# Kernel optimization log

Hardware: AMD Instinct MI355X
Metric: run time of the kernel (lower is better)

The kernel has to match this reference:

```python
import jax, jax.numpy as jnp
import numpy as np

NP_PEP, NP_PROT = 50000, 8000
E, EL = 1_600_000, 200_000
F_IN, H = 1280, 128


def _mean_aggr(x_src, src_idx, dst_idx, n_dst):
    # gather source feats per edge, scatter-mean into destination nodes
    msg = jax.ops.segment_sum(x_src[src_idx], dst_idx, num_segments=n_dst)  # [n_dst, H]
    deg = jax.ops.segment_sum(jnp.ones((src_idx.shape[0], 1), x_src.dtype), dst_idx, num_segments=n_dst)
    return msg / jnp.maximum(deg, 1.0)


def _hetero_sage(x_pep, x_prot, e_src, e_dst,
                 Wl_b, Wr_b, b_b, Wl_r, Wr_r, b_r):
    # edge type pep->prot (bind): updates prot nodes
    m_prot = _mean_aggr(x_pep, e_src, e_dst, x_prot.shape[0])
    out_prot = m_prot @ Wl_b + x_prot @ Wr_b + b_b
    # edge type prot->pep (rev_bind): updates pep nodes
    m_pep = _mean_aggr(x_prot, e_dst, e_src, x_pep.shape[0])
    out_pep = m_pep @ Wl_r + x_pep @ Wr_r + b_r
    return out_pep, out_prot


def setup_inputs() -> dict:
    key = jax.random.key(0)
    ks = jax.random.split(key, 24)
    s = 0.02
    inp = {
        'x_pep': jax.random.normal(ks[0], (NP_PEP, F_IN), jnp.float32),
        'x_prot': jax.random.normal(ks[1], (NP_PROT, F_IN), jnp.float32),
        'e_src': jax.random.randint(ks[2], (E,), 0, NP_PEP, jnp.int32),
        'e_dst': jax.random.randint(ks[3], (E,), 0, NP_PROT, jnp.int32),
        'el_src': jax.random.randint(ks[4], (EL,), 0, NP_PEP, jnp.int32),
        'el_dst': jax.random.randint(ks[5], (EL,), 0, NP_PROT, jnp.int32),
        'W_pep': s * jax.random.normal(ks[6], (F_IN, H), jnp.float32),
        'b_pep': jnp.zeros((H,), jnp.float32),
        'W_prot': s * jax.random.normal(ks[7], (F_IN, H), jnp.float32),
        'b_prot': jnp.zeros((H,), jnp.float32),
    }
    names = ['Wl1_bind', 'Wr1_bind', 'Wl1_rev', 'Wr1_rev',
             'Wl2_bind', 'Wr2_bind', 'Wl2_rev', 'Wr2_rev']
    for i, n in enumerate(names):
        inp[n] = s * jax.random.normal(ks[8 + i], (H, H), jnp.float32)
    for n in ['b1_bind', 'b1_rev', 'b2_bind', 'b2_rev']:
        inp[n] = jnp.zeros((H,), jnp.float32)
    return inp


def reference(x_pep, x_prot, e_src, e_dst, el_src, el_dst,
              W_pep, b_pep, W_prot, b_prot,
              Wl1_bind, Wr1_bind, b1_bind, Wl1_rev, Wr1_rev, b1_rev,
              Wl2_bind, Wr2_bind, b2_bind, Wl2_rev, Wr2_rev, b2_rev):
    # input projections (pep_emb/prot_emb unused in original forward)
    h_pep = x_pep @ W_pep + b_pep      # [NP_PEP, H]
    h_prot = x_prot @ W_prot + b_prot  # [NP_PROT, H]
    # SAGE layer 1 + relu
    h_pep, h_prot = _hetero_sage(h_pep, h_prot, e_src, e_dst,
                                 Wl1_bind, Wr1_bind, b1_bind,
                                 Wl1_rev, Wr1_rev, b1_rev)
    h_pep, h_prot = jax.nn.relu(h_pep), jax.nn.relu(h_prot)
    # SAGE layer 2
    h_pep, h_prot = _hetero_sage(h_pep, h_prot, e_src, e_dst,
                                 Wl2_bind, Wr2_bind, b2_bind,
                                 Wl2_rev, Wr2_rev, b2_rev)
    # classifier: edge-indexed gather + dot product
    return (h_pep[el_src] * h_prot[el_dst]).sum(axis=-1)  # [EL]
```

## Files before the change

### kernel.cpp

```cpp
#include <hip/hip_runtime.h>
#include <hip/hip_bf16.h>
#include <cstdint>

#define NP_PEP 50000
#define NP_PROT 8000
#define NE 1600000
#define NEL 200000
#define F_IN 1280
#define HDIM 128

#define CHUNK 4096
#define NBLK 391
#define NBQ 500
#define SHQ 4
#define NPBQ 16
#define NBP 391
#define SHP 7
#define NPBP 128

#define PROJ_BLK_PEP 391
#define PROJ_BLK_PROT 63
#define AGG_BLK_PROT 2000
#define AGG_BLK_PEP 12500

typedef __attribute__((ext_vector_type(8))) short bfrag;
typedef __attribute__((ext_vector_type(4))) short bhalf4;
typedef __attribute__((ext_vector_type(4))) float f32x4;

__device__ __forceinline__ ushort f2bf(float x) {
    __hip_bfloat16 h = __float2bfloat16(x);
    ushort u;
    __builtin_memcpy(&u, &h, 2);
    return u;
}
__device__ inline void unpack2(uint u, float& lo, float& hi) {
    union { uint u; float f; } a, b;
    a.u = u << 16; b.u = u & 0xffff0000u;
    lo = a.f; hi = b.f;
}
__device__ inline uint pack2(float a, float b) {
    return (uint)f2bf(a) | ((uint)f2bf(b) << 16);
}

__device__ __forceinline__ void cp16_g2l(const void* g, void* l) {
    __builtin_amdgcn_global_load_lds(
        (const __attribute__((address_space(1))) void*)g,
        (__attribute__((address_space(3))) void*)l, 16, 0, 0);
}


__global__ __launch_bounds__(512) void bin_count(const int* __restrict__ esrc,
                                                 const int* __restrict__ edst,
                                                 int* __restrict__ Gq,
                                                 int* __restrict__ Gp) {
    __shared__ int hq[NBQ];
    __shared__ int hp[NBP];
    int b = blockIdx.x, t = threadIdx.x;
    if (t < NBQ) hq[t] = 0;
    if (t < NBP) hp[t] = 0;
    __syncthreads();
    int e0 = b * CHUNK, cnt = min(CHUNK, NE - e0);
#pragma unroll
    for (int r = 0; r < 8; ++r) {
        int i = t + r * 512;
        if (i < cnt) {
            atomicAdd(&hq[edst[e0 + i] >> SHQ], 1);
            atomicAdd(&hp[esrc[e0 + i] >> SHP], 1);
        }
    }
    __syncthreads();
    if (t < NBQ) Gq[t * NBLK + b] = hq[t];
    if (t < NBP) Gp[t * NBLK + b] = hp[t];
}

__global__ __launch_bounds__(512) void rel_offsets(const int* __restrict__ Gq,
                                                   int* __restrict__ Oq, int* __restrict__ Tq,
                                                   const int* __restrict__ Gp,
                                                   int* __restrict__ Op, int* __restrict__ Tp) {
    const int* G; int* O; int* T; int j;
    if (blockIdx.x < NBQ) { G = Gq; O = Oq; T = Tq; j = blockIdx.x; }
    else                  { G = Gp; O = Op; T = Tp; j = blockIdx.x - NBQ; }
    __shared__ int sh[512];
    int t = threadIdx.x;
    int v = (t < NBLK) ? G[j * NBLK + t] : 0;
    sh[t] = v;
    __syncthreads();
    for (int off = 1; off < 512; off <<= 1) {
        int a = sh[t];
        int c = (t >= off) ? sh[t - off] : 0;
        __syncthreads();
        sh[t] = a + c;
        __syncthreads();
    }
    if (t < NBLK) O[j * NBLK + t] = sh[t] - v;
    if (t == 511) T[j] = sh[511];
}

__global__ __launch_bounds__(512) void base_scan(const int* __restrict__ Tq, int* __restrict__ Bq,
                                                 const int* __restrict__ Tp, int* __restrict__ Bp) {
    __shared__ int sh[512];
    int t = threadIdx.x;
    int v = (t < NBQ) ? Tq[t] : 0;
    sh[t] = v;
    __syncthreads();
    for (int off = 1; off < 512; off <<= 1) {
        int a = sh[t];
        int c = (t >= off) ? sh[t - off] : 0;
        __syncthreads();
        sh[t] = a + c;
        __syncthreads();
    }
    if (t < NBQ) Bq[t] = sh[t] - v;
    if (t == 0) Bq[NBQ] = NE;
    __syncthreads();
    int v2 = (t < NBP) ? Tp[t] : 0;
    sh[t] = v2;
    __syncthreads();
    for (int off = 1; off < 512; off <<= 1) {
        int a = sh[t];
        int c = (t >= off) ? sh[t - off] : 0;
        __syncthreads();
        sh[t] = a + c;
        __syncthreads();
    }
    if (t < NBP) Bp[t] = sh[t] - v2;
    if (t == 0) Bp[NBP] = NE;
}

__global__ __launch_bounds__(512) void bin_scatter2(const int* __restrict__ esrc,
                                                    const int* __restrict__ edst,
                                                    const int* __restrict__ Oq,
                                                    const int* __restrict__ Bq,
                                                    const int* __restrict__ Op,
                                                    const int* __restrict__ Bp,
                                                    uint* __restrict__ stagQ,
                                                    uint* __restrict__ stagP) {
    __shared__ int hist[512];
    __shared__ int start[512];
    __shared__ uint sorted[CHUNK];
    int b = blockIdx.x, t = threadIdx.x;
    int e0 = b * CHUNK, cnt = min(CHUNK, NE - e0);
    uint pk[8];
    bool val[8];
#pragma unroll
    for (int r = 0; r < 8; ++r) {
        int i = t + r * 512;
        val[r] = (i < cnt);
        if (val[r]) {
            int s = esrc[e0 + i], d = edst[e0 + i];
            pk[r] = ((uint)s << 13) | (uint)d;
        }
    }
    for (int dir = 0; dir < 2; ++dir) {
        const int* O = dir ? Op : Oq;
        const int* B = dir ? Bp : Bq;
        uint* stg = dir ? stagP : stagQ;
        int shf = dir ? SHP : SHQ;
        hist[t] = 0;
        __syncthreads();
        int bk[8];
#pragma unroll
        for (int r = 0; r < 8; ++r) {
            bk[r] = -1;
            if (val[r]) {
                int key = dir ? (int)(pk[r] >> 13) : (int)(pk[r] & 8191u);
                bk[r] = key >> shf;
                atomicAdd(&hist[bk[r]], 1);
            }
        }
        __syncthreads();
        int ownv = hist[t];
        start[t] = ownv;
        __syncthreads();
        for (int off = 1; off < 512; off <<= 1) {
            int a = start[t];
            int c = (t >= off) ? start[t - off] : 0;
            __syncthreads();
            start[t] = a + c;
            __syncthreads();
        }
        int excl = start[t] - ownv;
        start[t] = excl;
        hist[t] = excl;
        __syncthreads();
#pragma unroll
        for (int r = 0; r < 8; ++r)
            if (bk[r] >= 0) {
                int rank = atomicAdd(&hist[bk[r]], 1);
                sorted[rank] = pk[r];
            }
        __syncthreads();
#pragma unroll
        for (int r = 0; r < 8; ++r) {
            int i = t + r * 512;
            if (i < cnt) {
                uint v = sorted[i];
                int key = dir ? (int)(v >> 13) : (int)(v & 8191u);
                int bb = key >> shf;
                stg[B[bb] + O[bb * NBLK + b] + (i - start[bb])] = v;
            }
        }
        __syncthreads();
    }
}

__global__ __launch_bounds__(256) void finalize_csr(const uint* __restrict__ stagQ,
                                                    const int* __restrict__ Bq,
                                                    int* __restrict__ rowptr_prot,
                                                    int* __restrict__ col_prot,
                                                    const uint* __restrict__ stagP,
                                                    const int* __restrict__ Bp,
                                                    int* __restrict__ rowptr_pep,
                                                    int* __restrict__ col_pep) {
    __shared__ int cnts[128];
    __shared__ int sc[128];
    __shared__ int cur[128];
    const uint* stg; const int* B; int* rowptr; int* col;
    int n, npb, j, use_dst;
    if (blockIdx.x < NBQ) {
        stg = stagQ; B = Bq; rowptr = rowptr_prot; col = col_prot;
        n = NP_PROT; npb = NPBQ; j = blockIdx.x; use_dst = 1;
    } else {
        stg = stagP; B = Bp; rowptr = rowptr_pep; col = col_pep;
        n = NP_PEP; npb = NPBP; j = blockIdx.x - NBQ; use_dst = 0;
    }
    int t = threadIdx.x;
    int first = j * npb;
    int nn = min(npb, n - first);
    if (t < 128) cnts[t] = 0;
    __syncthreads();
    int s0 = B[j], s1 = B[j + 1];
    for (int i = s0 + t; i < s1; i += 256) {
        uint v = stg[i];
        int key = use_dst ? (int)(v & 8191u) : (int)(v >> 13);
        atomicAdd(&cnts[key - first], 1);
    }
    __syncthreads();
    int v = 0;
    if (t < 128) { v = cnts[t]; sc[t] = v; }
    __syncthreads();
    for (int off = 1; off < 128; off <<= 1) {
        int a = 0, c = 0;
        if (t < 128) { a = sc[t]; c = (t >= off) ? sc[t - off] : 0; }
        __syncthreads();
        if (t < 128) sc[t] = a + c;
        __syncthreads();
    }
    if (t < nn) {
        int excl = sc[t] - v;
        rowptr[first + t] = s0 + excl;
        cur[t] = s0 + excl;
    }
    if (t == 0 && j == 0) rowptr[n] = NE;
    __syncthreads();
    for (int i = s0 + t; i < s1; i += 256) {
        uint v2 = stg[i];
        int key, pay;
        if (use_dst) { key = (int)(v2 & 8191u); pay = (int)(v2 >> 13); }
        else         { key = (int)(v2 >> 13);   pay = (int)(v2 & 8191u); }
        int pos = atomicAdd(&cur[key - first], 1);
        col[pos] = pay;
    }
}


#define WST_TILE 4096

__global__ __launch_bounds__(256) void wprep(const float* __restrict__ Wp,
                                             const float* __restrict__ Wq,
                                             const float* __restrict__ m0,
                                             const float* __restrict__ m1,
                                             const float* __restrict__ m2,
                                             const float* __restrict__ m3,
                                             const float* __restrict__ m4,
                                             const float* __restrict__ m5,
                                             const float* __restrict__ m6,
                                             const float* __restrict__ m7,
                                             ushort* __restrict__ out) {
    int b = blockIdx.x;
    const float* W; int kt; size_t base;
    if (b < 40)      { W = Wp; kt = b;       base = 0; }
    else if (b < 80) { W = Wq; kt = b - 40;  base = (size_t)40 * WST_TILE; }
    else {
        int mm = (b - 80) >> 2; kt = (b - 80) & 3;
        switch (mm) {
            case 0: W = m0; break; case 1: W = m1; break;
            case 2: W = m2; break; case 3: W = m3; break;
            case 4: W = m4; break; case 5: W = m5; break;
            case 6: W = m6; break; default: W = m7; break;
        }
        base = (size_t)(80 + 4 * mm) * WST_TILE;
    }
    int t = threadIdx.x;
#pragma unroll
    for (int r = 0; r < 2; ++r) {
        int idx = t + r * 256;
        int n = ((idx >> 6) << 4) | (idx & 15);
        int h = (idx >> 4) & 3;
        const float* wp = W + (size_t)(kt * 32 + h * 8) * HDIM + n;
        bfrag p;
#pragma unroll
        for (int j = 0; j < 8; ++j) p[j] = (short)f2bf(wp[(size_t)j * HDIM]);
        *(bfrag*)&out[base + (size_t)kt * WST_TILE + (size_t)idx * 8] = p;
    }
}

__global__ __launch_bounds__(256) void gemm_proj2(const float* __restrict__ Aa,
                                                  const ushort* __restrict__ Wsta,
                                                  const float* __restrict__ ba,
                                                  ushort* __restrict__ Ca, int Ma, int nblk_a,
                                                  const float* __restrict__ Ab,
                                                  const ushort* __restrict__ Wstb,
                                                  const float* __restrict__ bb,
                                                  ushort* __restrict__ Cb, int Mb) {
    __shared__ ushort Alds[4096];
    __shared__ ushort Blds[4096];
    __shared__ ushort Clds[128 * 136];
    const float* A; const ushort* Wst; const float* bias; ushort* Cg; int M, blk;
    if ((int)blockIdx.x < nblk_a) { A = Aa; Wst = Wsta; bias = ba; Cg = Ca; M = Ma; blk = blockIdx.x; }
    else                          { A = Ab; Wst = Wstb; bias = bb; Cg = Cb; M = Mb; blk = blockIdx.x - nblk_a; }
    int tid = threadIdx.x;
    int lane = tid & 63, w = tid >> 6, wm = w >> 1, wn = w & 1;
    int r0 = blk * 128;

    f32x4 acc[4][4];
#pragma unroll
    for (int i = 0; i < 4; ++i)
#pragma unroll
        for (int j = 0; j < 4; ++j) acc[i][j] = (f32x4){0.f, 0.f, 0.f, 0.f};

    for (int kt = 0; kt < F_IN / 32; ++kt) {
        int k0 = kt * 32;
        const ushort* wsrc = Wst + (size_t)kt * WST_TILE;
        cp16_g2l(wsrc + (size_t)tid * 8, &Blds[(size_t)tid * 8]);
        cp16_g2l(wsrc + 2048 + (size_t)tid * 8, &Blds[2048 + (size_t)tid * 8]);
#pragma unroll
        for (int i = 0; i < 4; ++i) {
            int idx = tid + 256 * i;
            int row = idx >> 3, q = idx & 7;
            int gr = min(r0 + row, M - 1);
            float4 v = *(const float4*)(A + (size_t)gr * F_IN + k0 + q * 4);
            bhalf4 p;
            p.x = (short)f2bf(v.x); p.y = (short)f2bf(v.y);
            p.z = (short)f2bf(v.z); p.w = (short)f2bf(v.w);
            int off = ((row >> 4) * 64 + ((q >> 1) << 4) + (row & 15)) * 8 + (q & 1) * 4;
            *(bhalf4*)&Alds[off] = p;
        }
        __syncthreads();
        const bfrag* Af = (const bfrag*)Alds;
        const bfrag* Bf = (const bfrag*)Blds;
        bfrag af[4], bf_[4];
#pragma unroll
        for (int i = 0; i < 4; ++i) af[i] = Af[(wm * 4 + i) * 64 + lane];
#pragma unroll
        for (int j = 0; j < 4; ++j) bf_[j] = Bf[(wn * 4 + j) * 64 + lane];
#pragma unroll
        for (int i = 0; i < 4; ++i)
#pragma unroll
            for (int j = 0; j < 4; ++j)
                acc[i][j] = __builtin_amdgcn_mfma_f32_16x16x32_bf16(af[i], bf_[j], acc[i][j], 0, 0, 0);
        __syncthreads();
    }
#pragma unroll
    for (int j = 0; j < 4; ++j) {
        int colL = wn * 64 + j * 16 + (lane & 15);
        float bcol = bias[colL];
#pragma unroll
        for (int i = 0; i < 4; ++i) {
            int rbase = wm * 64 + i * 16 + ((lane >> 4) << 2);
            f32x4 v = acc[i][j];
            Clds[(rbase + 0) * 136 + colL] = f2bf(v.x + bcol);
            Clds[(rbase + 1) * 136 + colL] = f2bf(v.y + bcol);
            Clds[(rbase + 2) * 136 + colL] = f2bf(v.z + bcol);
            Clds[(rbase + 3) * 136 + colL] = f2bf(v.w + bcol);
        }
    }
    __syncthreads();
#pragma unroll
    for (int c = 0; c < 8; ++c) {
        int cidx = c * 256 + tid;
        int row = cidx >> 4, h = cidx & 15;
        int gr = r0 + row;
        if (gr < M)
            *(bfrag*)(Cg + (size_t)gr * HDIM + h * 8) = *(const bfrag*)&Clds[row * 136 + h * 8];
    }
}

__global__ __launch_bounds__(256) void lin2f(const ushort* A1a, const ushort* W1a,
                                             const ushort* A2a, const ushort* W2a,
                                             const float* __restrict__ ba,
                                             ushort* Ca, int Ma, int nblk_a,
                                             const ushort* A1b, const ushort* W1b,
                                             const ushort* A2b, const ushort* W2b,
                                             const float* __restrict__ bb,
                                             ushort* Cb, int Mb, int do_relu) {
    __shared__ ushort Alds[4096];
    __shared__ ushort Blds[4096];
    __shared__ ushort Clds[128 * 136];
    const ushort *A1, *A2, *W1, *W2; const float* bias; ushort* C; int M, blk;
    if ((int)blockIdx.x < nblk_a) {
        A1 = A1a; W1 = W1a; A2 = A2a; W2 = W2a; bias = ba; C = Ca; M = Ma; blk = blockIdx.x;
    } else {
        A1 = A1b; W1 = W1b; A2 = A2b; W2 = W2b; bias = bb; C = Cb; M = Mb; blk = blockIdx.x - nblk_a;
    }
    int tid = threadIdx.x;
    int lane = tid & 63, w = tid >> 6, wm = w >> 1, wn = w & 1;
    int r0 = blk * 128;

    int arow = ((tid >> 6) << 4) | (tid & 15);
    int ah = (tid >> 4) & 3;
    int gr1 = min(r0 + arow, M - 1);
    int gr2 = min(r0 + arow + 64, M - 1);

    f32x4 acc[4][4];
#pragma unroll
    for (int i = 0; i < 4; ++i)
#pragma unroll
        for (int j = 0; j < 4; ++j) acc[i][j] = (f32x4){0.f, 0.f, 0.f, 0.f};

    for (int kt = 0; kt < 8; ++kt) {
        const ushort* A = (kt < 4) ? A1 : A2;
        const ushort* Wt = (kt < 4) ? W1 : W2;
        int k0 = (kt & 3) * 32;
        cp16_g2l(A + (size_t)gr1 * HDIM + k0 + ah * 8, &Alds[(size_t)tid * 8]);
        cp16_g2l(A + (size_t)gr2 * HDIM + k0 + ah * 8, &Alds[(size_t)(tid + 256) * 8]);
        const ushort* wsrc = Wt + (size_t)(kt & 3) * WST_TILE;
        cp16_g2l(wsrc + (size_t)tid * 8, &Blds[(size_t)tid * 8]);
        cp16_g2l(wsrc + 2048 + (size_t)tid * 8, &Blds[2048 + (size_t)tid * 8]);
        __syncthreads();
        const bfrag* Af = (const bfrag*)Alds;
        const bfrag* Bf = (const bfrag*)Blds;
        bfrag af[4], bf_[4];
#pragma unroll
        for (int i = 0; i < 4; ++i) af[i] = Af[(wm * 4 + i) * 64 + lane];
#pragma unroll
        for (int j = 0; j < 4; ++j) bf_[j] = Bf[(wn * 4 + j) * 64 + lane];
#pragma unroll
        for (int i = 0; i < 4; ++i)
#pragma unroll
            for (int j = 0; j < 4; ++j)
                acc[i][j] = __builtin_amdgcn_mfma_f32_16x16x32_bf16(af[i], bf_[j], acc[i][j], 0, 0, 0);
        __syncthreads();
    }
#pragma unroll
    for (int j = 0; j < 4; ++j) {
        int colL = wn * 64 + j * 16 + (lane & 15);
        float bcol = bias[colL];
#pragma unroll
        for (int i = 0; i < 4; ++i) {
            int rbase = wm * 64 + i * 16 + ((lane >> 4) << 2);
            f32x4 v = acc[i][j];
            float o0 = v.x + bcol, o1 = v.y + bcol, o2 = v.z + bcol, o3 = v.w + bcol;
            if (do_relu) {
                o0 = fmaxf(o0, 0.f); o1 = fmaxf(o1, 0.f);
                o2 = fmaxf(o2, 0.f); o3 = fmaxf(o3, 0.f);
            }
            Clds[(rbase + 0) * 136 + colL] = f2bf(o0);
            Clds[(rbase + 1) * 136 + colL] = f2bf(o1);
            Clds[(rbase + 2) * 136 + colL] = f2bf(o2);
            Clds[(rbase + 3) * 136 + colL] = f2bf(o3);
        }
    }
    __syncthreads();
#pragma unroll
    for (int c = 0; c < 8; ++c) {
        int cidx = c * 256 + tid;
        int row = cidx >> 4, h = cidx & 15;
        int gr = r0 + row;
        if (gr < M)
            *(bfrag*)(C + (size_t)gr * HDIM + h * 8) = *(const bfrag*)&Clds[row * 136 + h * 8];
    }
}

__global__ __launch_bounds__(256) void aggr2(const ushort* __restrict__ Ha,
                                             const int* __restrict__ rpa,
                                             const int* __restrict__ cola,
                                             ushort* __restrict__ Oa, int Na, int nblk_a,
                                             const ushort* __restrict__ Hb,
                                             const int* __restrict__ rpb,
                                             const int* __restrict__ colb,
                                             ushort* __restrict__ Ob, int Nb) {
    const ushort* H; const int* rp; const int* col; ushort* O; int N, blk;
    if ((int)blockIdx.x < nblk_a) { H = Ha; rp = rpa; col = cola; O = Oa; N = Na; blk = blockIdx.x; }
    else                          { H = Hb; rp = rpb; col = colb; O = Ob; N = Nb; blk = blockIdx.x - nblk_a; }
    int node = blk * 4 + (threadIdx.x >> 6);
    if (node >= N) return;
    int lane = threadIdx.x & 63;
    int sub = lane >> 4;
    int ch = lane & 15;
    int beg = rp[node], end = rp[node + 1];
    int deg = end - beg;
    float a0 = 0, a1 = 0, a2 = 0, a3 = 0, a4 = 0, a5 = 0, a6 = 0, a7 = 0;
    int j = beg + sub;
    for (; j + 4 < end; j += 8) {
        int i0 = col[j], i1 = col[j + 4];
        uint4 u0 = *(const uint4*)(H + (size_t)i0 * HDIM + ch * 8);
        uint4 u1 = *(const uint4*)(H + (size_t)i1 * HDIM + ch * 8);
        float lo, hi;
        unpack2(u0.x, lo, hi); a0 += lo; a1 += hi;
        unpack2(u0.y, lo, hi); a2 += lo; a3 += hi;
        unpack2(u0.z, lo, hi); a4 += lo; a5 += hi;
        unpack2(u0.w, lo, hi); a6 += lo; a7 += hi;
        unpack2(u1.x, lo, hi); a0 += lo; a1 += hi;
        unpack2(u1.y, lo, hi); a2 += lo; a3 += hi;
        unpack2(u1.z, lo, hi); a4 += lo; a5 += hi;
        unpack2(u1.w, lo, hi); a6 += lo; a7 += hi;
    }
    if (j < end) {
        int i0 = col[j];
        uint4 u0 = *(const uint4*)(H + (size_t)i0 * HDIM + ch * 8);
        float lo, hi;
        unpack2(u0.x, lo, hi); a0 += lo; a1 += hi;
        unpack2(u0.y, lo, hi); a2 += lo; a3 += hi;
        unpack2(u0.z, lo, hi); a4 += lo; a5 += hi;
        unpack2(u0.w, lo, hi); a6 += lo; a7 += hi;
    }
    a0 += __shfl_xor(a0, 16); a0 += __shfl_xor(a0, 32);
    a1 += __shfl_xor(a1, 16); a1 += __shfl_xor(a1, 32);
    a2 += __shfl_xor(a2, 16); a2 += __shfl_xor(a2, 32);
    a3 += __shfl_xor(a3, 16); a3 += __shfl_xor(a3, 32);
    a4 += __shfl_xor(a4, 16); a4 += __shfl_xor(a4, 32);
    a5 += __shfl_xor(a5, 16); a5 += __shfl_xor(a5, 32);
    a6 += __shfl_xor(a6, 16); a6 += __shfl_xor(a6, 32);
    a7 += __shfl_xor(a7, 16); a7 += __shfl_xor(a7, 32);
    if (sub == 0) {
        float inv = 1.0f / (float)max(deg, 1);
        uint4 o;
        o.x = pack2(a0 * inv, a1 * inv);
        o.y = pack2(a2 * inv, a3 * inv);
        o.z = pack2(a4 * inv, a5 * inv);
        o.w = pack2(a6 * inv, a7 * inv);
        *(uint4*)(O + (size_t)node * HDIM + ch * 8) = o;
    }
}

__global__ __launch_bounds__(256) void classify_bf16(const ushort* __restrict__ hp,
                                                     const ushort* __restrict__ hr,
                                                     const int* __restrict__ esrc,
                                                     const int* __restrict__ edst,
                                                     float* __restrict__ out, int n) {
    int t = blockIdx.x * blockDim.x + threadIdx.x;
    int edge = t >> 4;
    int ch = t & 15;
    if (edge >= n) return;
    int s = esrc[edge], d = edst[edge];
    uint4 ua = *(const uint4*)(hp + (size_t)s * HDIM + ch * 8);
    uint4 ub = *(const uint4*)(hr + (size_t)d * HDIM + ch * 8);
    float al, ah, bl, bh;
    float v = 0.f;
    unpack2(ua.x, al, ah); unpack2(ub.x, bl, bh); v += al * bl + ah * bh;
    unpack2(ua.y, al, ah); unpack2(ub.y, bl, bh); v += al * bl + ah * bh;
    unpack2(ua.z, al, ah); unpack2(ub.z, bl, bh); v += al * bl + ah * bh;
    unpack2(ua.w, al, ah); unpack2(ub.w, bl, bh); v += al * bl + ah * bh;
    v += __shfl_xor(v, 8);
    v += __shfl_xor(v, 4);
    v += __shfl_xor(v, 2);
    v += __shfl_xor(v, 1);
    if (ch == 0) out[edge] = v;
}


extern "C" void kernel_launch(void* const* d_in, const int* in_sizes, int n_in,
                              void* d_out, int out_size, void* d_ws, size_t ws_size,
                              hipStream_t stream) {
    const float* x_pep   = (const float*)d_in[0];
    const float* x_prot  = (const float*)d_in[1];
    const int*   e_src   = (const int*)d_in[2];
    const int*   e_dst   = (const int*)d_in[3];
    const int*   el_src  = (const int*)d_in[4];
    const int*   el_dst  = (const int*)d_in[5];
    const float* W_pep   = (const float*)d_in[6];
    const float* b_pep   = (const float*)d_in[7];
    const float* W_prot  = (const float*)d_in[8];
    const float* b_prot  = (const float*)d_in[9];
    const float* Wl1_bind = (const float*)d_in[10];
    const float* Wr1_bind = (const float*)d_in[11];
    const float* Wl1_rev  = (const float*)d_in[12];
    const float* Wr1_rev  = (const float*)d_in[13];
    const float* Wl2_bind = (const float*)d_in[14];
    const float* Wr2_bind = (const float*)d_in[15];
    const float* Wl2_rev  = (const float*)d_in[16];
    const float* Wr2_rev  = (const float*)d_in[17];
    const float* b1_bind  = (const float*)d_in[18];
    const float* b1_rev   = (const float*)d_in[19];
    const float* b2_bind  = (const float*)d_in[20];
    const float* b2_rev   = (const float*)d_in[21];
    float* out = (float*)d_out;

    ushort* P0 = (ushort*)d_ws;
    ushort* P1 = P0 + (size_t)NP_PEP * HDIM;
    ushort* R0 = P1 + (size_t)NP_PEP * HDIM;
    ushort* R1 = R0 + (size_t)NP_PROT * HDIM;
    int* rowptr_pep  = (int*)(R1 + (size_t)NP_PROT * HDIM);
    int* rowptr_prot = rowptr_pep + NP_PEP + 1;
    int* col_pep     = rowptr_prot + NP_PROT + 1;
    int* col_prot    = col_pep + NE;
    uint* stagP      = (uint*)(col_prot + NE);
    uint* stagQ      = stagP + NE;
    int* Gq          = (int*)(stagQ + NE);
    int* Oq          = Gq + NBQ * NBLK;
    int* Gp          = Oq + NBQ * NBLK;
    int* Op          = Gp + NBP * NBLK;
    int* Tq          = Op + NBP * NBLK;
    int* Tp          = Tq + NBQ;
    int* Bq          = Tp + NBP;
    int* Bp          = Bq + NBQ + 1;
    uintptr_t wraw   = (uintptr_t)(Bp + NBP + 1);
    ushort* Wst      = (ushort*)((wraw + 255) & ~(uintptr_t)255);

    const ushort* WstPep  = Wst;
    const ushort* WstProt = Wst + (size_t)40 * WST_TILE;
    const ushort* WstL1b  = Wst + (size_t)(80 + 0)  * WST_TILE;
    const ushort* WstR1b  = Wst + (size_t)(80 + 4)  * WST_TILE;
    const ushort* WstL1r  = Wst + (size_t)(80 + 8)  * WST_TILE;
    const ushort* WstR1r  = Wst + (size_t)(80 + 12) * WST_TILE;
    const ushort* WstL2b  = Wst + (size_t)(80 + 16) * WST_TILE;
    const ushort* WstR2b  = Wst + (size_t)(80 + 20) * WST_TILE;
    const ushort* WstL2r  = Wst + (size_t)(80 + 24) * WST_TILE;
    const ushort* WstR2r  = Wst + (size_t)(80 + 28) * WST_TILE;

    wprep<<<112, 256, 0, stream>>>(W_pep, W_prot,
                                   Wl1_bind, Wr1_bind, Wl1_rev, Wr1_rev,
                                   Wl2_bind, Wr2_bind, Wl2_rev, Wr2_rev, Wst);

    bin_count<<<NBLK, 512, 0, stream>>>(e_src, e_dst, Gq, Gp);
    rel_offsets<<<NBQ + NBP, 512, 0, stream>>>(Gq, Oq, Tq, Gp, Op, Tp);
    base_scan<<<1, 512, 0, stream>>>(Tq, Bq, Tp, Bp);
    bin_scatter2<<<NBLK, 512, 0, stream>>>(e_src, e_dst, Oq, Bq, Op, Bp, stagQ, stagP);
    finalize_csr<<<NBQ + NBP, 256, 0, stream>>>(stagQ, Bq, rowptr_prot, col_prot,
                                                stagP, Bp, rowptr_pep, col_pep);

    gemm_proj2<<<PROJ_BLK_PEP + PROJ_BLK_PROT, 256, 0, stream>>>(
        x_pep, WstPep, b_pep, P0, NP_PEP, PROJ_BLK_PEP,
        x_prot, WstProt, b_prot, R0, NP_PROT);

    aggr2<<<AGG_BLK_PROT + AGG_BLK_PEP, 256, 0, stream>>>(
        P0, rowptr_prot, col_prot, R1, NP_PROT, AGG_BLK_PROT,
        R0, rowptr_pep, col_pep, P1, NP_PEP);
    lin2f<<<PROJ_BLK_PEP + PROJ_BLK_PROT, 256, 0, stream>>>(
        P1, WstL1r, P0, WstR1r, b1_rev, P1, NP_PEP, PROJ_BLK_PEP,
        R1, WstL1b, R0, WstR1b, b1_bind, R1, NP_PROT, 1);

    aggr2<<<AGG_BLK_PROT + AGG_BLK_PEP, 256, 0, stream>>>(
        P1, rowptr_prot, col_prot, R0, NP_PROT, AGG_BLK_PROT,
        R1, rowptr_pep, col_pep, P0, NP_PEP);
    lin2f<<<PROJ_BLK_PEP + PROJ_BLK_PROT, 256, 0, stream>>>(
        P0, WstL2r, P1, WstR2r, b2_rev, P0, NP_PEP, PROJ_BLK_PEP,
        R0, WstL2b, R1, WstR2b, b2_bind, R0, NP_PROT, 0);

    classify_bf16<<<(NEL * 16 + 255) / 256, 256, 0, stream>>>(P0, R0, el_src, el_dst, out, NEL);
}
```

Baseline: 664.8 us.

## Fuse weight prep into bin count, projection into CSR finalize, use wave-shuffle scans

Merges the weight conversion kernel into the edge bin-count launch and the input projection GEMM into the CSR finalize launch, so independent work shares one grid and two launches disappear. Replaces the LDS Hillis-Steele scans, which need many barriers, with wave-level shuffle scans plus a small cross-wave fixup. Unrolls the aggregation gather loop to 16 edges per step so more loads are in flight. The fused kernels carry the larger shared-memory footprint of the GEMM into the CSR blocks, which may reduce occupancy.

Measured after the change: 636.3 us. -4.3%, faster.

```diff
diff --git a/kernel.cpp b/kernel.cpp
--- a/kernel.cpp
+++ b/kernel.cpp
@@ -20,6 +20,7 @@
 
 #define PROJ_BLK_PEP 391
 #define PROJ_BLK_PROT 63
+#define PROJ_TOT (PROJ_BLK_PEP + PROJ_BLK_PROT)
 #define AGG_BLK_PROT 2000
 #define AGG_BLK_PEP 12500
 
@@ -48,14 +49,61 @@
         (__attribute__((address_space(3))) void*)l, 16, 0, 0);
 }
 
-
-__global__ __launch_bounds__(512) void bin_count(const int* __restrict__ esrc,
-                                                 const int* __restrict__ edst,
-                                                 int* __restrict__ Gq,
-                                                 int* __restrict__ Gp) {
+__device__ __forceinline__ int wscan_incl(int x) {
+#pragma unroll
+    for (int d = 1; d < 64; d <<= 1) {
+        int y = __shfl_up(x, d);
+        if ((int)(threadIdx.x & 63) >= d) x += y;
+    }
+    return x;
+}
+
+#define WST_TILE 4096
+
+__global__ __launch_bounds__(512) void prep_count(const int* __restrict__ esrc,
+                                                  const int* __restrict__ edst,
+                                                  int* __restrict__ Gq,
+                                                  int* __restrict__ Gp,
+                                                  const float* __restrict__ Wp,
+                                                  const float* __restrict__ Wq,
+                                                  const float* __restrict__ m0,
+                                                  const float* __restrict__ m1,
+                                                  const float* __restrict__ m2,
+                                                  const float* __restrict__ m3,
+                                                  const float* __restrict__ m4,
+                                                  const float* __restrict__ m5,
+                                                  const float* __restrict__ m6,
+                                                  const float* __restrict__ m7,
+                                                  ushort* __restrict__ wout) {
+    int b = blockIdx.x;
+    if (b >= NBLK) {
+        int bb = b - NBLK;
+        const float* W; int kt; size_t base;
+        if (bb < 40)      { W = Wp; kt = bb;       base = 0; }
+        else if (bb < 80) { W = Wq; kt = bb - 40;  base = (size_t)40 * WST_TILE; }
+        else {
+            int mm = (bb - 80) >> 2; kt = (bb - 80) & 3;
+            switch (mm) {
+                case 0: W = m0; break; case 1: W = m1; break;
+                case 2: W = m2; break; case 3: W = m3; break;
+                case 4: W = m4; break; case 5: W = m5; break;
+                case 6: W = m6; break; default: W = m7; break;
+            }
+            base = (size_t)(80 + 4 * mm) * WST_TILE;
+        }
+        int idx = threadIdx.x;
+        int n = ((idx >> 6) << 4) | (idx & 15);
+        int h = (idx >> 4) & 3;
+        const float* wp = W + (size_t)(kt * 32 + h * 8) * HDIM + n;
+        bfrag p;
+#pragma unroll
+        for (int j = 0; j < 8; ++j) p[j] = (short)f2bf(wp[(size_t)j * HDIM]);
+        *(bfrag*)&wout[base + (size_t)kt * WST_TILE + (size_t)idx * 8] = p;
+        return;
+    }
     __shared__ int hq[NBQ];
     __shared__ int hp[NBP];
-    int b = blockIdx.x, t = threadIdx.x;
+    int t = threadIdx.x;
     if (t < NBQ) hq[t] = 0;
     if (t < NBP) hp[t] = 0;
     __syncthreads();
@@ -80,50 +128,49 @@
     const int* G; int* O; int* T; int j;
     if (blockIdx.x < NBQ) { G = Gq; O = Oq; T = Tq; j = blockIdx.x; }
     else                  { G = Gp; O = Op; T = Tp; j = blockIdx.x - NBQ; }
-    __shared__ int sh[512];
+    __shared__ int wsum[8];
     int t = threadIdx.x;
+    int lane = t & 63, wid = t >> 6;
     int v = (t < NBLK) ? G[j * NBLK + t] : 0;
-    sh[t] = v;
-    __syncthreads();
-    for (int off = 1; off < 512; off <<= 1) {
-        int a = sh[t];
-        int c = (t >= off) ? sh[t - off] : 0;
-        __syncthreads();
-        sh[t] = a + c;
-        __syncthreads();
-    }
-    if (t < NBLK) O[j * NBLK + t] = sh[t] - v;
-    if (t == 511) T[j] = sh[511];
+    int inc = wscan_incl(v);
+    if (lane == 63) wsum[wid] = inc;
+    __syncthreads();
+    int add = 0;
+#pragma unroll
+    for (int w = 0; w < 7; ++w)
+        if (w < wid) add += wsum[w];
+    inc += add;
+    if (t < NBLK) O[j * NBLK + t] = inc - v;
+    if (t == 511) T[j] = inc;
 }
 
 __global__ __launch_bounds__(512) void base_scan(const int* __restrict__ Tq, int* __restrict__ Bq,
                                                  const int* __restrict__ Tp, int* __restrict__ Bp) {
-    __shared__ int sh[512];
+    __shared__ int wsum[8];
     int t = threadIdx.x;
+    int lane = t & 63, wid = t >> 6;
     int v = (t < NBQ) ? Tq[t] : 0;
-    sh[t] = v;
-    __syncthreads();
-    for (int off = 1; off < 512; off <<= 1) {
-        int a = sh[t];
-        int c = (t >= off) ? sh[t - off] : 0;
-        __syncthreads();
-        sh[t] = a + c;
-        __syncthreads();
-    }
-    if (t < NBQ) Bq[t] = sh[t] - v;
+    int inc = wscan_incl(v);
+    if (lane == 63) wsum[wid] = inc;
+    __syncthreads();
+    int add = 0;
+#pragma unroll
+    for (int w = 0; w < 7; ++w)
+        if (w < wid) add += wsum[w];
+    inc += add;
+    if (t < NBQ) Bq[t] = inc - v;
     if (t == 0) Bq[NBQ] = NE;
     __syncthreads();
     int v2 = (t < NBP) ? Tp[t] : 0;
-    sh[t] = v2;
-    __syncthreads();
-    for (int off = 1; off < 512; off <<= 1) {
-        int a = sh[t];
-        int c = (t >= off) ? sh[t - off] : 0;
-        __syncthreads();
-        sh[t] = a + c;
-        __syncthreads();
-    }
-    if (t < NBP) Bp[t] = sh[t] - v2;
+    int inc2 = wscan_incl(v2);
+    if (lane == 63) wsum[wid] = inc2;
+    __syncthreads();
+    add = 0;
+#pragma unroll
+    for (int w = 0; w < 7; ++w)
+        if (w < wid) add += wsum[w];
+    inc2 += add;
+    if (t < NBP) Bp[t] = inc2 - v2;
     if (t == 0) Bp[NBP] = NE;
 }
 
@@ -138,7 +185,9 @@
     __shared__ int hist[512];
     __shared__ int start[512];
     __shared__ uint sorted[CHUNK];
+    __shared__ int wsum[8];
     int b = blockIdx.x, t = threadIdx.x;
+    int lane = t & 63, wid = t >> 6;
     int e0 = b * CHUNK, cnt = min(CHUNK, NE - e0);
     uint pk[8];
     bool val[8];
@@ -170,16 +219,14 @@
         }
         __syncthreads();
         int ownv = hist[t];
-        start[t] = ownv;
-        __syncthreads();
-        for (int off = 1; off < 512; off <<= 1) {
-            int a = start[t];
-            int c = (t >= off) ? start[t - off] : 0;
-            __syncthreads();
-            start[t] = a + c;
-            __syncthreads();
-        }
-        int excl = start[t] - ownv;
+        int inc = wscan_incl(ownv);
+        if (lane == 63) wsum[wid] = inc;
+        __syncthreads();
+        int add = 0;
+#pragma unroll
+        for (int w = 0; w < 7; ++w)
+            if (w < wid) add += wsum[w];
+        int excl = inc + add - ownv;
         start[t] = excl;
         hist[t] = excl;
         __syncthreads();
@@ -204,27 +251,104 @@
     }
 }
 
-__global__ __launch_bounds__(256) void finalize_csr(const uint* __restrict__ stagQ,
-                                                    const int* __restrict__ Bq,
-                                                    int* __restrict__ rowptr_prot,
-                                                    int* __restrict__ col_prot,
-                                                    const uint* __restrict__ stagP,
-                                                    const int* __restrict__ Bp,
-                                                    int* __restrict__ rowptr_pep,
-                                                    int* __restrict__ col_pep) {
-    __shared__ int cnts[128];
-    __shared__ int sc[128];
-    __shared__ int cur[128];
+__global__ __launch_bounds__(256) void proj_fincsr(
+    const float* __restrict__ Aa, const ushort* __restrict__ Wsta,
+    const float* __restrict__ ba, ushort* __restrict__ Ca, int Ma,
+    const float* __restrict__ Ab, const ushort* __restrict__ Wstb,
+    const float* __restrict__ bb_, ushort* __restrict__ Cb, int Mb,
+    const uint* __restrict__ stagQ, const int* __restrict__ Bq,
+    int* __restrict__ rowptr_prot, int* __restrict__ col_prot,
+    const uint* __restrict__ stagP, const int* __restrict__ Bp,
+    int* __restrict__ rowptr_pep, int* __restrict__ col_pep) {
+    __shared__ ushort Alds[4096];
+    __shared__ ushort Blds[4096];
+    __shared__ ushort Clds[128 * 136];
+    int bx = blockIdx.x;
+    int tid = threadIdx.x;
+    if (bx < PROJ_TOT) {
+        const float* A; const ushort* Wst; const float* bias; ushort* Cg; int M, blk;
+        if (bx < PROJ_BLK_PEP) { A = Aa; Wst = Wsta; bias = ba; Cg = Ca; M = Ma; blk = bx; }
+        else                   { A = Ab; Wst = Wstb; bias = bb_; Cg = Cb; M = Mb; blk = bx - PROJ_BLK_PEP; }
+        int lane = tid & 63, w = tid >> 6, wm = w >> 1, wn = w & 1;
+        int r0 = blk * 128;
+
+        f32x4 acc[4][4];
+#pragma unroll
+        for (int i = 0; i < 4; ++i)
+#pragma unroll
+            for (int j = 0; j < 4; ++j) acc[i][j] = (f32x4){0.f, 0.f, 0.f, 0.f};
+
+        for (int kt = 0; kt < F_IN / 32; ++kt) {
+            int k0 = kt * 32;
+            const ushort* wsrc = Wst + (size_t)kt * WST_TILE;
+            cp16_g2l(wsrc + (size_t)tid * 8, &Blds[(size_t)tid * 8]);
+            cp16_g2l(wsrc + 2048 + (size_t)tid * 8, &Blds[2048 + (size_t)tid * 8]);
+#pragma unroll
+            for (int i = 0; i < 4; ++i) {
+                int idx = tid + 256 * i;
+                int row = idx >> 3, q = idx & 7;
+                int gr = min(r0 + row, M - 1);
+                float4 v = *(const float4*)(A + (size_t)gr * F_IN + k0 + q * 4);
+                bhalf4 p;
+                p.x = (short)f2bf(v.x); p.y = (short)f2bf(v.y);
+                p.z = (short)f2bf(v.z); p.w = (short)f2bf(v.w);
+                int off = ((row >> 4) * 64 + ((q >> 1) << 4) + (row & 15)) * 8 + (q & 1) * 4;
+                *(bhalf4*)&Alds[off] = p;
+            }
+            __syncthreads();
+            const bfrag* Af = (const bfrag*)Alds;
+            const bfrag* Bf = (const bfrag*)Blds;
+            bfrag af[4], bf_[4];
+#pragma unroll
+            for (int i = 0; i < 4; ++i) af[i] = Af[(wm * 4 + i) * 64 + lane];
+#pragma unroll
+            for (int j = 0; j < 4; ++j) bf_[j] = Bf[(wn * 4 + j) * 64 + lane];
+#pragma unroll
+            for (int i = 0; i < 4; ++i)
+#pragma unroll
+                for (int j = 0; j < 4; ++j)
+                    acc[i][j] = __builtin_amdgcn_mfma_f32_16x16x32_bf16(af[i], bf_[j], acc[i][j], 0, 0, 0);
+            __syncthreads();
+        }
+#pragma unroll
+        for (int j = 0; j < 4; ++j) {
+            int colL = wn * 64 + j * 16 + (lane & 15);
+            float bcol = bias[colL];
+#pragma unroll
+            for (int i = 0; i < 4; ++i) {
+                int rbase = wm * 64 + i * 16 + ((lane >> 4) << 2);
+                f32x4 v = acc[i][j];
+                Clds[(rbase + 0) * 136 + colL] = f2bf(v.x + bcol);
+                Clds[(rbase + 1) * 136 + colL] = f2bf(v.y + bcol);
+                Clds[(rbase + 2) * 136 + colL] = f2bf(v.z + bcol);
+                Clds[(rbase + 3) * 136 + colL] = f2bf(v.w + bcol);
+            }
+        }
+        __syncthreads();
+#pragma unroll
+        for (int c = 0; c < 8; ++c) {
+            int cidx = c * 256 + tid;
+            int row = cidx >> 4, h = cidx & 15;
+            int gr = r0 + row;
+            if (gr < M)
+                *(bfrag*)(Cg + (size_t)gr * HDIM + h * 8) = *(const bfrag*)&Clds[row * 136 + h * 8];
+        }
+        return;
+    }
+    int fb = bx - PROJ_TOT;
+    int* cnts = (int*)Alds;
+    int* cur  = cnts + 128;
+    int* wsf  = cur + 128;
     const uint* stg; const int* B; int* rowptr; int* col;
     int n, npb, j, use_dst;
-    if (blockIdx.x < NBQ) {
+    if (fb < NBQ) {
         stg = stagQ; B = Bq; rowptr = rowptr_prot; col = col_prot;
-        n = NP_PROT; npb = NPBQ; j = blockIdx.x; use_dst = 1;
+        n = NP_PROT; npb = NPBQ; j = fb; use_dst = 1;
     } else {
         stg = stagP; B = Bp; rowptr = rowptr_pep; col = col_pep;
-        n = NP_PEP; npb = NPBP; j = blockIdx.x - NBQ; use_dst = 0;
-    }
-    int t = threadIdx.x;
+        n = NP_PEP; npb = NPBP; j = fb - NBQ; use_dst = 0;
+    }
+    int t = tid;
     int first = j * npb;
     int nn = min(npb, n - first);
     if (t < 128) cnts[t] = 0;
@@ -236,19 +360,14 @@
         atomicAdd(&cnts[key - first], 1);
     }
     __syncthreads();
-    int v = 0;
-    if (t < 128) { v = cnts[t]; sc[t] = v; }
-    __syncthreads();
-    for (int off = 1; off < 128; off <<= 1) {
-        int a = 0, c = 0;
-        if (t < 128) { a = sc[t]; c = (t >= off) ? sc[t - off] : 0; }
-        __syncthreads();
-        if (t < 128) sc[t] = a + c;
-        __syncthreads();
-    }
-    if (t < nn) {
-        int excl = sc[t] - v;
-        rowptr[first + t] = s0 + excl;
+    int v = (t < 128) ? cnts[t] : 0;
+    int inc = wscan_incl(v);
+    if (t == 63) wsf[0] = inc;
+    __syncthreads();
+    if (t >= 64 && t < 128) inc += wsf[0];
+    if (t < 128) {
+        int excl = inc - v;
+        if (t < nn) rowptr[first + t] = s0 + excl;
         cur[t] = s0 + excl;
     }
     if (t == 0 && j == 0) rowptr[n] = NE;
@@ -260,129 +379,6 @@
         else         { key = (int)(v2 >> 13);   pay = (int)(v2 & 8191u); }
         int pos = atomicAdd(&cur[key - first], 1);
         col[pos] = pay;
-    }
-}
-
-
-#define WST_TILE 4096
-
-__global__ __launch_bounds__(256) void wprep(const float* __restrict__ Wp,
-                                             const float* __restrict__ Wq,
-                                             const float* __restrict__ m0,
-                                             const float* __restrict__ m1,
-                                             const float* __restrict__ m2,
-                                             const float* __restrict__ m3,
-                                             const float* __restrict__ m4,
-                                             const float* __restrict__ m5,
-                                             const float* __restrict__ m6,
-                                             const float* __restrict__ m7,
-                                             ushort* __restrict__ out) {
-    int b = blockIdx.x;
-    const float* W; int kt; size_t base;
-    if (b < 40)      { W = Wp; kt = b;       base = 0; }
-    else if (b < 80) { W = Wq; kt = b - 40;  base = (size_t)40 * WST_TILE; }
-    else {
-        int mm = (b - 80) >> 2; kt = (b - 80) & 3;
-        switch (mm) {
-            case 0: W = m0; break; case 1: W = m1; break;
-            case 2: W = m2; break; case 3: W = m3; break;
-            case 4: W = m4; break; case 5: W = m5; break;
-            case 6: W = m6; break; default: W = m7; break;
-        }
-        base = (size_t)(80 + 4 * mm) * WST_TILE;
-    }
-    int t = threadIdx.x;
-#pragma unroll
-    for (int r = 0; r < 2; ++r) {
-        int idx = t + r * 256;
-        int n = ((idx >> 6) << 4) | (idx & 15);
-        int h = (idx >> 4) & 3;
-        const float* wp = W + (size_t)(kt * 32 + h * 8) * HDIM + n;
-        bfrag p;
-#pragma unroll
-        for (int j = 0; j < 8; ++j) p[j] = (short)f2bf(wp[(size_t)j * HDIM]);
-        *(bfrag*)&out[base + (size_t)kt * WST_TILE + (size_t)idx * 8] = p;
-    }
-}
-
-__global__ __launch_bounds__(256) void gemm_proj2(const float* __restrict__ Aa,
-                                                  const ushort* __restrict__ Wsta,
-                                                  const float* __restrict__ ba,
-                                                  ushort* __restrict__ Ca, int Ma, int nblk_a,
-                                                  const float* __restrict__ Ab,
-                                                  const ushort* __restrict__ Wstb,
-                                                  const float* __restrict__ bb,
-                                                  ushort* __restrict__ Cb, int Mb) {
-    __shared__ ushort Alds[4096];
-    __shared__ ushort Blds[4096];
-    __shared__ ushort Clds[128 * 136];
-    const float* A; const ushort* Wst; const float* bias; ushort* Cg; int M, blk;
-    if ((int)blockIdx.x < nblk_a) { A = Aa; Wst = Wsta; bias = ba; Cg = Ca; M = Ma; blk = blockIdx.x; }
-    else                          { A = Ab; Wst = Wstb; bias = bb; Cg = Cb; M = Mb; blk = blockIdx.x - nblk_a; }
-    int tid = threadIdx.x;
-    int lane = tid & 63, w = tid >> 6, wm = w >> 1, wn = w & 1;
-    int r0 = blk * 128;
-
-    f32x4 acc[4][4];
-#pragma unroll
-    for (int i = 0; i < 4; ++i)
-#pragma unroll
-        for (int j = 0; j < 4; ++j) acc[i][j] = (f32x4){0.f, 0.f, 0.f, 0.f};
-
-    for (int kt = 0; kt < F_IN / 32; ++kt) {
-        int k0 = kt * 32;
-        const ushort* wsrc = Wst + (size_t)kt * WST_TILE;
-        cp16_g2l(wsrc + (size_t)tid * 8, &Blds[(size_t)tid * 8]);
-        cp16_g2l(wsrc + 2048 + (size_t)tid * 8, &Blds[2048 + (size_t)tid * 8]);
-#pragma unroll
-        for (int i = 0; i < 4; ++i) {
-            int idx = tid + 256 * i;
-            int row = idx >> 3, q = idx & 7;
-            int gr = min(r0 + row, M - 1);
-            float4 v = *(const float4*)(A + (size_t)gr * F_IN + k0 + q * 4);
-            bhalf4 p;
-            p.x = (short)f2bf(v.x); p.y = (short)f2bf(v.y);
-            p.z = (short)f2bf(v.z); p.w = (short)f2bf(v.w);
-            int off = ((row >> 4) * 64 + ((q >> 1) << 4) + (row & 15)) * 8 + (q & 1) * 4;
-            *(bhalf4*)&Alds[off] = p;
-        }
-        __syncthreads();
-        const bfrag* Af = (const bfrag*)Alds;
-        const bfrag* Bf = (const bfrag*)Blds;
-        bfrag af[4], bf_[4];
-#pragma unroll
-        for (int i = 0; i < 4; ++i) af[i] = Af[(wm * 4 + i) * 64 + lane];
-#pragma unroll
-        for (int j = 0; j < 4; ++j) bf_[j] = Bf[(wn * 4 + j) * 64 + lane];
-#pragma unroll
-        for (int i = 0; i < 4; ++i)
-#pragma unroll
-            for (int j = 0; j < 4; ++j)
-                acc[i][j] = __builtin_amdgcn_mfma_f32_16x16x32_bf16(af[i], bf_[j], acc[i][j], 0, 0, 0);
-        __syncthreads();
-    }
-#pragma unroll
-    for (int j = 0; j < 4; ++j) {
-        int colL = wn * 64 + j * 16 + (lane & 15);
-        float bcol = bias[colL];
-#pragma unroll
-        for (int i = 0; i < 4; ++i) {
-            int rbase = wm * 64 + i * 16 + ((lane >> 4) << 2);
-            f32x4 v = acc[i][j];
-            Clds[(rbase + 0) * 136 + colL] = f2bf(v.x + bcol);
-            Clds[(rbase + 1) * 136 + colL] = f2bf(v.y + bcol);
-            Clds[(rbase + 2) * 136 + colL] = f2bf(v.z + bcol);
-            Clds[(rbase + 3) * 136 + colL] = f2bf(v.w + bcol);
-        }
-    }
-    __syncthreads();
-#pragma unroll
-    for (int c = 0; c < 8; ++c) {
-        int cidx = c * 256 + tid;
-        int row = cidx >> 4, h = cidx & 15;
-        int gr = r0 + row;
-        if (gr < M)
-            *(bfrag*)(Cg + (size_t)gr * HDIM + h * 8) = *(const bfrag*)&Clds[row * 136 + h * 8];
     }
 }
 
@@ -492,6 +488,30 @@
     int deg = end - beg;
     float a0 = 0, a1 = 0, a2 = 0, a3 = 0, a4 = 0, a5 = 0, a6 = 0, a7 = 0;
     int j = beg + sub;
+    for (; j + 12 < end; j += 16) {
+        int i0 = col[j], i1 = col[j + 4], i2 = col[j + 8], i3 = col[j + 12];
+        uint4 u0 = *(const uint4*)(H + (size_t)i0 * HDIM + ch * 8);
+        uint4 u1 = *(const uint4*)(H + (size_t)i1 * HDIM + ch * 8);
+        uint4 u2 = *(const uint4*)(H + (size_t)i2 * HDIM + ch * 8);
+        uint4 u3 = *(const uint4*)(H + (size_t)i3 * HDIM + ch * 8);
+        float lo, hi;
+        unpack2(u0.x, lo, hi); a0 += lo; a1 += hi;
+        unpack2(u0.y, lo, hi); a2 += lo; a3 += hi;
+        unpack2(u0.z, lo, hi); a4 += lo; a5 += hi;
+        unpack2(u0.w, lo, hi); a6 += lo; a7 += hi;
+        unpack2(u1.x, lo, hi); a0 += lo; a1 += hi;
+        unpack2(u1.y, lo, hi); a2 += lo; a3 += hi;
+        unpack2(u1.z, lo, hi); a4 += lo; a5 += hi;
+        unpack2(u1.w, lo, hi); a6 += lo; a7 += hi;
+        unpack2(u2.x, lo, hi); a0 += lo; a1 += hi;
+        unpack2(u2.y, lo, hi); a2 += lo; a3 += hi;
+        unpack2(u2.z, lo, hi); a4 += lo; a5 += hi;
+        unpack2(u2.w, lo, hi); a6 += lo; a7 += hi;
+        unpack2(u3.x, lo, hi); a0 += lo; a1 += hi;
+        unpack2(u3.y, lo, hi); a2 += lo; a3 += hi;
+        unpack2(u3.z, lo, hi); a4 += lo; a5 += hi;
+        unpack2(u3.w, lo, hi); a6 += lo; a7 += hi;
+    }
     for (; j + 4 < end; j += 8) {
         int i0 = col[j], i1 = col[j + 4];
         uint4 u0 = *(const uint4*)(H + (size_t)i0 * HDIM + ch * 8);
@@ -619,20 +639,19 @@
     const ushort* WstL2r  = Wst + (size_t)(80 + 24) * WST_TILE;
     const ushort* WstR2r  = Wst + (size_t)(80 + 28) * WST_TILE;
 
-    wprep<<<112, 256, 0, stream>>>(W_pep, W_prot,
-                                   Wl1_bind, Wr1_bind, Wl1_rev, Wr1_rev,
-                                   Wl2_bind, Wr2_bind, Wl2_rev, Wr2_rev, Wst);
-
-    bin_count<<<NBLK, 512, 0, stream>>>(e_src, e_dst, Gq, Gp);
+    prep_count<<<NBLK + 112, 512, 0, stream>>>(e_src, e_dst, Gq, Gp,
+                                               W_pep, W_prot,
+                                               Wl1_bind, Wr1_bind, Wl1_rev, Wr1_rev,
+                                               Wl2_bind, Wr2_bind, Wl2_rev, Wr2_rev, Wst);
     rel_offsets<<<NBQ + NBP, 512, 0, stream>>>(Gq, Oq, Tq, Gp, Op, Tp);
     base_scan<<<1, 512, 0, stream>>>(Tq, Bq, Tp, Bp);
     bin_scatter2<<<NBLK, 512, 0, stream>>>(e_src, e_dst, Oq, Bq, Op, Bp, stagQ, stagP);
-    finalize_csr<<<NBQ + NBP, 256, 0, stream>>>(stagQ, Bq, rowptr_prot, col_prot,
-                                                stagP, Bp, rowptr_pep, col_pep);
-
-    gemm_proj2<<<PROJ_BLK_PEP + PROJ_BLK_PROT, 256, 0, stream>>>(
-        x_pep, WstPep, b_pep, P0, NP_PEP, PROJ_BLK_PEP,
-        x_prot, WstProt, b_prot, R0, NP_PROT);
+
+    proj_fincsr<<<PROJ_TOT + NBQ + NBP, 256, 0, stream>>>(
+        x_pep, WstPep, b_pep, P0, NP_PEP,
+        x_prot, WstProt, b_prot, R0, NP_PROT,
+        stagQ, Bq, rowptr_prot, col_prot,
+        stagP, Bp, rowptr_pep, col_pep);
 
     aggr2<<<AGG_BLK_PROT + AGG_BLK_PEP, 256, 0, stream>>>(
         P0, rowptr_prot, col_prot, R1, NP_PROT, AGG_BLK_PROT,
```
